# Kernel tuning notes

Measured on AMD Instinct MI355X. Metric: run time of the kernel, lower is better.

The kernel has to match this reference:

```python
import jax, jax.numpy as jnp
import numpy as np
from jax import lax

STRIDE = 1
PAD = 1


def setup_inputs() -> dict:
    key = jax.random.key(0)
    k1, k2 = jax.random.split(key)
    X = jax.random.normal(k1, (16, 64, 256, 256), dtype=jnp.float32)
    K = jax.random.normal(k2, (3, 3), dtype=jnp.float32)
    return {"X": X, "K": K}


def reference(X, K):
    # out[b, c, i, j] = sum(patch(X[b, c], i, j) * K)
    # == depthwise conv with a single shared 2D kernel for all channels.
    B, C, H, W = X.shape
    x = X.reshape(B * C, 1, H, W)            # fold channels into batch
    k = K[None, None, :, :]                  # [O=1, I=1, kh, kw]
    out = lax.conv_general_dilated(
        x, k,
        window_strides=(STRIDE, STRIDE),
        padding=[(PAD, PAD), (PAD, PAD)],
        dimension_numbers=("NCHW", "OIHW", "NCHW"),
    )
    Ho, Wo = out.shape[2], out.shape[3]
    return out.reshape(B, C, Ho, Wo)
```

## Files before the change

kernel.cpp:

```cpp
#include <hip/hip_runtime.h>


#define CONV_H 256
#define CONV_W 256
#define CONV_W4 64
#define NPLANES (16 * 64)
#define ROWS_PER_THREAD 8
#define STRIPES (CONV_H / ROWS_PER_THREAD)
#define PDEPTH 4

typedef float v4f __attribute__((ext_vector_type(4)));

struct Row { float4 c; float l, r; };

__device__ __forceinline__ Row expand_row(float4 c, int lane, float valid) {
    Row v;
    float l = __shfl_up(c.w, 1);
    float r = __shfl_down(c.x, 1);
    v.c.x = c.x * valid;
    v.c.y = c.y * valid;
    v.c.z = c.z * valid;
    v.c.w = c.w * valid;
    v.l = (lane == 0)  ? 0.f : l * valid;
    v.r = (lane == 63) ? 0.f : r * valid;
    return v;
}

__global__ __launch_bounds__(256)
void conv3x3_kernel(const float* __restrict__ X,
                    const float* __restrict__ Kw,
                    float* __restrict__ out)
{
    const float k00 = Kw[0], k01 = Kw[1], k02 = Kw[2];
    const float k10 = Kw[3], k11 = Kw[4], k12 = Kw[5];
    const float k20 = Kw[6], k21 = Kw[7], k22 = Kw[8];

    const int chunk = gridDim.x >> 3;
    const int lb = (blockIdx.x & 7) * chunk + (blockIdx.x >> 3);

    const int tid    = lb * blockDim.x + threadIdx.x;
    const int lane   = threadIdx.x & 63;
    const int w4     = tid & (CONV_W4 - 1);
    const int stripe = tid >> 6;
    const int h0     = (stripe & (STRIPES - 1)) << 3;
    const int p      = stripe >> 5;

    const float* colp = X + (size_t)p * (CONV_H * CONV_W) + (w4 << 2);
    float* outp = out + (size_t)p * (CONV_H * CONV_W)
                      + (size_t)h0 * CONV_W + (w4 << 2);

    float4 raw[PDEPTH];
    #pragma unroll
    for (int j = 0; j < PDEPTH; ++j) {
        int r   = h0 - 1 + j;
        int rcl = min(max(r, 0), CONV_H - 1);
        raw[j] = *(const float4*)(colp + rcl * CONV_W);
    }

    Row rm = expand_row(raw[0], lane, (h0 > 0) ? 1.f : 0.f);
    Row rc = expand_row(raw[1], lane, 1.f);

    #pragma unroll
    for (int i = 0; i < ROWS_PER_THREAD; ++i) {
        if (i < ROWS_PER_THREAD - 2) {
            int r   = h0 + PDEPTH - 1 + i;
            int rcl = min(r, CONV_H - 1);
            raw[i & (PDEPTH - 1)] = *(const float4*)(colp + rcl * CONV_W);
        }

        const int rpr = h0 + 1 + i;
        Row rp = expand_row(raw[(i + 2) & (PDEPTH - 1)], lane,
                            (rpr < CONV_H) ? 1.f : 0.f);

        float4 o;
        o.x = k00 * rm.l   + k01 * rm.c.x + k02 * rm.c.y
            + k10 * rc.l   + k11 * rc.c.x + k12 * rc.c.y
            + k20 * rp.l   + k21 * rp.c.x + k22 * rp.c.y;
        o.y = k00 * rm.c.x + k01 * rm.c.y + k02 * rm.c.z
            + k10 * rc.c.x + k11 * rc.c.y + k12 * rc.c.z
            + k20 * rp.c.x + k21 * rp.c.y + k22 * rp.c.z;
        o.z = k00 * rm.c.y + k01 * rm.c.z + k02 * rm.c.w
            + k10 * rc.c.y + k11 * rc.c.z + k12 * rc.c.w
            + k20 * rp.c.y + k21 * rp.c.z + k22 * rp.c.w;
        o.w = k00 * rm.c.z + k01 * rm.c.w + k02 * rm.r
            + k10 * rc.c.z + k11 * rc.c.w + k12 * rc.r
            + k20 * rp.c.z + k21 * rp.c.w + k22 * rp.r;

        v4f ov = { o.x, o.y, o.z, o.w };
        __builtin_nontemporal_store(ov, (v4f*)(outp + i * CONV_W));

        rm = rc;
        rc = rp;
    }
}

extern "C" void kernel_launch(void* const* d_in, const int* in_sizes, int n_in,
                              void* d_out, int out_size, void* d_ws, size_t ws_size,
                              hipStream_t stream) {
    const float* X  = (const float*)d_in[0];
    const float* Kw = (const float*)d_in[1];
    float* out = (float*)d_out;

    const int total_threads = NPLANES * STRIPES * CONV_W4;
    const int block = 256;
    const int grid = total_threads / block;
    conv3x3_kernel<<<grid, block, 0, stream>>>(X, Kw, out);
}
```

Measured before the change: 442.7 us.

## Assign one plane per block with 64-row stripes per wave and deeper prefetch

Each block now processes a whole 256x256 plane, with each 64-lane wave covering a 64-row stripe instead of 8 rows. A rolling register prefetch ring of depth 8 replaces the old depth 4. This cuts the halo-row overhead from 2 extra rows per 8 to 2 per 64 and drops the XCD-aware block remapping. In exchange the grid is much smaller (1024 blocks) and there is less parallelism, so latency hiding now rests on the per-thread prefetch ring.

```diff
diff --git a/kernel.cpp b/kernel.cpp
--- a/kernel.cpp
+++ b/kernel.cpp
@@ -3,11 +3,9 @@
 
 #define CONV_H 256
 #define CONV_W 256
-#define CONV_W4 64
 #define NPLANES (16 * 64)
-#define ROWS_PER_THREAD 8
-#define STRIPES (CONV_H / ROWS_PER_THREAD)
-#define PDEPTH 4
+#define ROWS 64
+#define DEPTH 8
 
 typedef float v4f __attribute__((ext_vector_type(4)));
 
@@ -35,23 +33,18 @@
     const float k10 = Kw[3], k11 = Kw[4], k12 = Kw[5];
     const float k20 = Kw[6], k21 = Kw[7], k22 = Kw[8];
 
-    const int chunk = gridDim.x >> 3;
-    const int lb = (blockIdx.x & 7) * chunk + (blockIdx.x >> 3);
+    const int lane    = threadIdx.x & 63;
+    const int quarter = threadIdx.x >> 6;
+    const int p       = blockIdx.x;
+    const int h0      = quarter << 6;
 
-    const int tid    = lb * blockDim.x + threadIdx.x;
-    const int lane   = threadIdx.x & 63;
-    const int w4     = tid & (CONV_W4 - 1);
-    const int stripe = tid >> 6;
-    const int h0     = (stripe & (STRIPES - 1)) << 3;
-    const int p      = stripe >> 5;
+    const float* colp = X   + (size_t)p * (CONV_H * CONV_W) + (lane << 2);
+    float*       outp = out + (size_t)p * (CONV_H * CONV_W)
+                            + (size_t)h0 * CONV_W + (lane << 2);
 
-    const float* colp = X + (size_t)p * (CONV_H * CONV_W) + (w4 << 2);
-    float* outp = out + (size_t)p * (CONV_H * CONV_W)
-                      + (size_t)h0 * CONV_W + (w4 << 2);
-
-    float4 raw[PDEPTH];
+    float4 raw[DEPTH];
     #pragma unroll
-    for (int j = 0; j < PDEPTH; ++j) {
+    for (int j = 0; j < DEPTH; ++j) {
         int r   = h0 - 1 + j;
         int rcl = min(max(r, 0), CONV_H - 1);
         raw[j] = *(const float4*)(colp + rcl * CONV_W);
@@ -60,37 +53,39 @@
     Row rm = expand_row(raw[0], lane, (h0 > 0) ? 1.f : 0.f);
     Row rc = expand_row(raw[1], lane, 1.f);
 
-    #pragma unroll
-    for (int i = 0; i < ROWS_PER_THREAD; ++i) {
-        if (i < ROWS_PER_THREAD - 2) {
-            int r   = h0 + PDEPTH - 1 + i;
-            int rcl = min(r, CONV_H - 1);
-            raw[i & (PDEPTH - 1)] = *(const float4*)(colp + rcl * CONV_W);
+    const int rowcap = min(h0 + ROWS + 1, CONV_H - 1);
+
+    for (int ii = 0; ii < ROWS; ii += DEPTH) {
+        #pragma unroll
+        for (int j = 0; j < DEPTH; ++j) {
+            const int i = ii + j;
+            int pr = min(h0 + DEPTH - 1 + i, rowcap);
+            raw[j] = *(const float4*)(colp + pr * CONV_W);
+
+            const int rpr = h0 + 1 + i;
+            Row rp = expand_row(raw[(j + 2) & (DEPTH - 1)], lane,
+                                (rpr < CONV_H) ? 1.f : 0.f);
+
+            float4 o;
+            o.x = k00 * rm.l   + k01 * rm.c.x + k02 * rm.c.y
+                + k10 * rc.l   + k11 * rc.c.x + k12 * rc.c.y
+                + k20 * rp.l   + k21 * rp.c.x + k22 * rp.c.y;
+            o.y = k00 * rm.c.x + k01 * rm.c.y + k02 * rm.c.z
+                + k10 * rc.c.x + k11 * rc.c.y + k12 * rc.c.z
+                + k20 * rp.c.x + k21 * rp.c.y + k22 * rp.c.z;
+            o.z = k00 * rm.c.y + k01 * rm.c.z + k02 * rm.c.w
+                + k10 * rc.c.y + k11 * rc.c.z + k12 * rc.c.w
+                + k20 * rp.c.y + k21 * rp.c.z + k22 * rp.c.w;
+            o.w = k00 * rm.c.z + k01 * rm.c.w + k02 * rm.r
+                + k10 * rc.c.z + k11 * rc.c.w + k12 * rc.r
+                + k20 * rp.c.z + k21 * rp.c.w + k22 * rp.r;
+
+            v4f ov = { o.x, o.y, o.z, o.w };
+            __builtin_nontemporal_store(ov, (v4f*)(outp + i * CONV_W));
+
+            rm = rc;
+            rc = rp;
         }
-
-        const int rpr = h0 + 1 + i;
-        Row rp = expand_row(raw[(i + 2) & (PDEPTH - 1)], lane,
-                            (rpr < CONV_H) ? 1.f : 0.f);
-
-        float4 o;
-        o.x = k00 * rm.l   + k01 * rm.c.x + k02 * rm.c.y
-            + k10 * rc.l   + k11 * rc.c.x + k12 * rc.c.y
-            + k20 * rp.l   + k21 * rp.c.x + k22 * rp.c.y;
-        o.y = k00 * rm.c.x + k01 * rm.c.y + k02 * rm.c.z
-            + k10 * rc.c.x + k11 * rc.c.y + k12 * rc.c.z
-            + k20 * rp.c.x + k21 * rp.c.y + k22 * rp.c.z;
-        o.z = k00 * rm.c.y + k01 * rm.c.z + k02 * rm.c.w
-            + k10 * rc.c.y + k11 * rc.c.z + k12 * rc.c.w
-            + k20 * rp.c.y + k21 * rp.c.z + k22 * rp.c.w;
-        o.w = k00 * rm.c.z + k01 * rm.c.w + k02 * rm.r
-            + k10 * rc.c.z + k11 * rc.c.w + k12 * rc.r
-            + k20 * rp.c.z + k21 * rp.c.w + k22 * rp.r;
-
-        v4f ov = { o.x, o.y, o.z, o.w };
-        __builtin_nontemporal_store(ov, (v4f*)(outp + i * CONV_W));
-
-        rm = rc;
-        rc = rp;
     }
 }
 
@@ -101,8 +96,5 @@
     const float* Kw = (const float*)d_in[1];
     float* out = (float*)d_out;
 
-    const int total_threads = NPLANES * STRIPES * CONV_W4;
-    const int block = 256;
-    const int grid = total_threads / block;
-    conv3x3_kernel<<<grid, block, 0, stream>>>(X, Kw, out);
+    conv3x3_kernel<<<NPLANES, 256, 0, stream>>>(X, Kw, out);
 }
```

New measurement: 456.0 us. 3.0% more time.
